# Optimization experiments

Hardware: AMD Instinct MI355X
Metric: run time of the kernel (lower is better)

Reference implementation:

```python
import jax, jax.numpy as jnp
import numpy as np

# dims
B, NV, C, HF, WF = 2, 4, 64, 128, 232
NX, NY, NZ = 128, 128, 8
VRANGE = (-25.6, -25.6, -1.0, 25.6, 25.6, 3.0)
EPS = 1e-5


def _voxel_points():
    # voxel-center grid, ordered so that reshape(NZ, NY, NX, C) is valid (x fastest)
    dx = (VRANGE[3] - VRANGE[0]) / NX
    dy = (VRANGE[4] - VRANGE[1]) / NY
    dz = (VRANGE[5] - VRANGE[2]) / NZ
    xs = VRANGE[0] + dx * (jnp.arange(NX, dtype=jnp.float32) + 0.5)
    ys = VRANGE[1] + dy * (jnp.arange(NY, dtype=jnp.float32) + 0.5)
    zs = VRANGE[2] + dz * (jnp.arange(NZ, dtype=jnp.float32) + 0.5)
    zg, yg, xg = jnp.meshgrid(zs, ys, xs, indexing='ij')  # [NZ,NY,NX]
    return jnp.stack([xg, yg, zg], axis=-1).reshape(-1, 3)  # [N,3]


def _make_cameras():
    # 4 outward-facing cameras (front, left, back, right) in a lidar frame (x fwd, y left, z up)
    dirs = [(1.0, 0.0, 0.0), (0.0, 1.0, 0.0), (-1.0, 0.0, 0.0), (0.0, -1.0, 0.0)]
    up = np.array([0.0, 0.0, 1.0])
    l2c = np.zeros((NV, 4, 4), np.float32)
    for v, f in enumerate(dirs):
        f = np.array(f)
        xc = np.cross(f, up); xc /= np.linalg.norm(xc)  # cam right
        yc = np.cross(f, xc)                              # cam down
        R = np.stack([xc, yc, f], axis=0)                 # rows: x_c, y_c, z_c
        pos = 1.0 * f + np.array([0.0, 0.0, 1.5])
        l2c[v, :3, :3] = R
        l2c[v, :3, 3] = -R @ pos
        l2c[v, 3, 3] = 1.0
    # intrinsics directly in feature-map pixel scale
    fx = fy = 0.5 * WF
    K = np.array([[fx, 0.0, WF / 2.0], [0.0, fy, HF / 2.0], [0.0, 0.0, 1.0]], np.float32)
    cam2img = np.broadcast_to(K, (NV, 3, 3))
    return (np.broadcast_to(l2c, (B, NV, 4, 4)).copy(),
            np.broadcast_to(cam2img, (B, NV, 3, 3)).copy())


def setup_inputs() -> dict:
    key = jax.random.key(0)
    feats = jax.random.normal(key, (B, NV, C, HF, WF), dtype=jnp.float32)
    l2c, k = _make_cameras()
    return {"feats": feats, "lidar2cam": jnp.asarray(l2c), "cam2img": jnp.asarray(k)}


def _bilinear(feat, px, py):
    # feat: [C,H,W]; px,py: [N] sample coords (grid_sample align_corners=False => shift by 0.5)
    x = px - 0.5
    y = py - 0.5
    x0 = jnp.floor(x); y0 = jnp.floor(y)
    wx = x - x0; wy = y - y0
    x0i = x0.astype(jnp.int32); y0i = y0.astype(jnp.int32)

    def gather(xi, yi):
        inb = (xi >= 0) & (xi < WF) & (yi >= 0) & (yi < HF)
        xc = jnp.clip(xi, 0, WF - 1)
        yc = jnp.clip(yi, 0, HF - 1)
        return feat[:, yc, xc] * inb[None, :].astype(feat.dtype)  # [C,N]

    return (gather(x0i, y0i) * ((1 - wx) * (1 - wy))[None]
            + gather(x0i + 1, y0i) * (wx * (1 - wy))[None]
            + gather(x0i, y0i + 1) * ((1 - wx) * wy)[None]
            + gather(x0i + 1, y0i + 1) * (wx * wy)[None])


def reference(feats, lidar2cam, cam2img):
    pts = _voxel_points()                                   # [N,3]
    pts_h = jnp.concatenate([pts, jnp.ones((pts.shape[0], 1), pts.dtype)], axis=-1)  # [N,4]
    cam = jnp.einsum('bvij,nj->bvni', lidar2cam, pts_h)[..., :3]  # [B,NV,N,3]
    z = cam[..., 2]
    uvw = jnp.einsum('bvij,bvnj->bvni', cam2img, cam)
    zc = jnp.clip(z, EPS, None)
    px = uvw[..., 0] / zc
    py = uvw[..., 1] / zc
    valid = (z > EPS) & (px >= 0) & (px < WF) & (py >= 0) & (py < HF)  # [B,NV,N]

    sample = jax.vmap(jax.vmap(_bilinear))(feats, px, py)   # [B,NV,C,N]
    sample = sample * valid[:, :, None, :].astype(sample.dtype)

    vol = sample.sum(axis=1)                                 # [B,C,N] sum over views
    cnt = valid.astype(jnp.float32).sum(axis=1)              # [B,N]
    vol = vol / jnp.clip(cnt, 1.0, None)[:, None, :]         # mean over valid views (0 where none)

    # [B,C,N] -> [N,C]-style reshape(NZ,NY,NX,C).permute(3,2,1,0) per sample -> [B,C,NX,NY,NZ]
    vol = vol.transpose(0, 2, 1).reshape(B, NZ, NY, NX, C)
    vol = vol.transpose(0, 4, 3, 2, 1)                       # [B,C,NX,NY,NZ]
    return vol
```

## Files before the change

kernel.cpp:

```cpp
#include <hip/hip_runtime.h>

#define BB   2
#define NVV  4
#define CC   64
#define HFF  128
#define WFF  232
#define HW   (HFF*WFF)
#define EPSV 1e-5f

__global__ __launch_bounds__(256) void transpose_kernel(
    const float* __restrict__ feats, float* __restrict__ ft)
{
    __shared__ float lds[64][65];
    const int t   = threadIdx.x;
    const int hw0 = blockIdx.x * 64;
    const size_t sbase = (size_t)blockIdx.y * (CC * HW);

    const int lhw = t & 63, crow = t >> 6;
#pragma unroll
    for (int r = 0; r < 16; ++r) {
        const int c = crow * 16 + r;
        lds[c][lhw] = feats[sbase + (size_t)c * HW + hw0 + lhw];
    }
    __syncthreads();
    const int lc = t & 63, hrow = t >> 6;
#pragma unroll
    for (int r = 0; r < 16; ++r) {
        const int hw = hrow + 4 * r;
        ft[sbase + (size_t)(hw0 + hw) * CC + lc] = lds[lc][hw];
    }
}

__global__ __launch_bounds__(256) void bev_sample_kernel(
    const float* __restrict__ ft,
    const float* __restrict__ l2c,
    const float* __restrict__ cam2img,
    float* __restrict__ out)
{
    __shared__ __align__(16) char smem[16640];
    int4*   s_off = (int4*)smem;
    float4* s_w   = (float4*)(smem + 4096);
    int*    s_fl  = (int*)(smem + 8192);
    float*  s_t   = (float*)smem;

    const int t   = threadIdx.x;
    const int bid = blockIdx.x;
    const int b   = bid >> 11;
    const int rem = bid & 2047;
    const int xi  = rem >> 4;
    const int yz0 = (rem & 15) << 6;

    {
        const int v = t >> 6, j = t & 63;
        const int yzi = yz0 + j;
        const int yi = yzi >> 3, zi = yzi & 7;
        const float X = -25.6f + 0.4f * ((float)xi + 0.5f);
        const float Y = -25.6f + 0.4f * ((float)yi + 0.5f);
        const float Z = -1.0f  + 0.5f * ((float)zi + 0.5f);

        const float* M = l2c + ((b * NVV + v) << 4);
        const float* K = cam2img + (b * NVV + v) * 9;
        const float cx = fmaf(M[0], X, fmaf(M[1], Y, fmaf(M[2],  Z, M[3])));
        const float cy = fmaf(M[4], X, fmaf(M[5], Y, fmaf(M[6],  Z, M[7])));
        const float cz = fmaf(M[8], X, fmaf(M[9], Y, fmaf(M[10], Z, M[11])));
        const float u = fmaf(K[0], cx, fmaf(K[1], cy, K[2] * cz));
        const float w = fmaf(K[3], cx, fmaf(K[4], cy, K[5] * cz));
        const float zc = fmaxf(cz, EPSV);
        const float rz = 1.f / zc;
        const float px = u * rz, py = w * rz;

        const bool valid = (cz > EPSV) && (px >= 0.f) && (px < (float)WFF)
                         && (py >= 0.f) && (py < (float)HFF);

        const float xf = px - 0.5f, yf = py - 0.5f;
        const float x0f = floorf(xf), y0f = floorf(yf);
        const float wx = xf - x0f, wy = yf - y0f;
        const int x0 = (int)x0f, y0 = (int)y0f;
        const int x1 = x0 + 1, y1 = y0 + 1;
        const bool bx0 = (x0 >= 0) & (x0 < WFF);
        const bool bx1 = (x1 >= 0) & (x1 < WFF);
        const bool by0 = (y0 >= 0) & (y0 < HFF);
        const bool by1 = (y1 >= 0) & (y1 < HFF);
        float4 wt;
        wt.x = (bx0 && by0) ? (1.f - wx) * (1.f - wy) : 0.f;
        wt.y = (bx1 && by0) ? wx * (1.f - wy)         : 0.f;
        wt.z = (bx0 && by1) ? (1.f - wx) * wy         : 0.f;
        wt.w = (bx1 && by1) ? wx * wy                 : 0.f;
        const int x0c = min(max(x0, 0), WFF-1), x1c = min(max(x1, 0), WFF-1);
        const int y0c = min(max(y0, 0), HFF-1), y1c = min(max(y1, 0), HFF-1);
        int4 off;
        off.x = y0c*WFF + x0c; off.y = y0c*WFF + x1c;
        off.z = y1c*WFF + x0c; off.w = y1c*WFF + x1c;

        s_off[v*64 + j] = off;
        s_w  [v*64 + j] = wt;
        ((char*)(smem + 8192))[j*4 + v] = valid ? 1 : 0;
    }
    __syncthreads();

    const int wv = t >> 6, c = t & 63;
    float acc[16];
#pragma unroll
    for (int k = 0; k < 16; ++k) acc[k] = 0.f;

    const float* fslice0 = ft + (size_t)(b * NVV) * (HW * CC);
#pragma unroll
    for (int k = 0; k < 16; ++k) {
        const int j = wv*16 + k;
        const int flags = s_fl[j];
        const int cnt = (flags & 1) + ((flags >> 8) & 1)
                      + ((flags >> 16) & 1) + ((flags >> 24) & 1);
        float a = 0.f;
#pragma unroll
        for (int v = 0; v < NVV; ++v) {
            if ((flags >> (8*v)) & 1) {
                const int4   off = s_off[v*64 + j];
                const float4 wt  = s_w  [v*64 + j];
                const float* fb  = fslice0 + (size_t)v * (HW * CC);
                a = fmaf(fb[(size_t)off.x*CC + c], wt.x, a);
                a = fmaf(fb[(size_t)off.y*CC + c], wt.y, a);
                a = fmaf(fb[(size_t)off.z*CC + c], wt.z, a);
                a = fmaf(fb[(size_t)off.w*CC + c], wt.w, a);
            }
        }
        const float scale = (cnt <= 1) ? 1.f : (cnt == 2) ? 0.5f
                          : (cnt == 3) ? (1.f/3.f) : 0.25f;
        acc[k] = a * scale;
    }
    __syncthreads();

#pragma unroll
    for (int k = 0; k < 16; ++k)
        s_t[(wv*16 + k)*65 + c] = acc[k];
    __syncthreads();

    const int jv = t & 63, cr = t >> 6;
    float* ob = out + (size_t)b * (CC * 131072) + (size_t)xi * 1024 + yz0;
#pragma unroll
    for (int r = 0; r < 16; ++r) {
        const int c2 = cr + 4*r;
        ob[(size_t)c2 * 131072 + jv] = s_t[jv*65 + c2];
    }
}

#define CG 16
__global__ __launch_bounds__(256) void bev_fuse_kernel(
    const float* __restrict__ feats, const float* __restrict__ l2c,
    const float* __restrict__ cam2img, float* __restrict__ out)
{
    const int tid = blockIdx.x * 256 + threadIdx.x;
    const int b   = tid >> 17;
    const int rem = tid & 131071;
    const int xi  = rem >> 10;
    const int yzi = rem & 1023;
    const int yi  = yzi >> 3;
    const int zi  = yzi & 7;
    const int c0  = blockIdx.y * CG;

    const float X = -25.6f + 0.4f * ((float)xi + 0.5f);
    const float Y = -25.6f + 0.4f * ((float)yi + 0.5f);
    const float Z = -1.0f  + 0.5f * ((float)zi + 0.5f);

    float acc[CG];
#pragma unroll
    for (int c = 0; c < CG; ++c) acc[c] = 0.f;
    float cnt = 0.f;

    for (int v = 0; v < NVV; ++v) {
        const float* M = l2c + ((b * NVV + v) << 4);
        const float* K = cam2img + (b * NVV + v) * 9;
        const float cx = fmaf(M[0], X, fmaf(M[1], Y, fmaf(M[2],  Z, M[3])));
        const float cy = fmaf(M[4], X, fmaf(M[5], Y, fmaf(M[6],  Z, M[7])));
        const float cz = fmaf(M[8], X, fmaf(M[9], Y, fmaf(M[10], Z, M[11])));
        const float u = fmaf(K[0], cx, fmaf(K[1], cy, K[2] * cz));
        const float w = fmaf(K[3], cx, fmaf(K[4], cy, K[5] * cz));
        const float zc = fmaxf(cz, EPSV);
        const float rz = 1.f / zc;
        const float px = u * rz, py = w * rz;
        const bool valid = (cz > EPSV) && (px >= 0.f) && (px < (float)WFF)
                         && (py >= 0.f) && (py < (float)HFF);
        if (!valid) continue;
        cnt += 1.f;
        const float xf = px - 0.5f, yf = py - 0.5f;
        const float x0f = floorf(xf), y0f = floorf(yf);
        const float wx = xf - x0f, wy = yf - y0f;
        const int x0 = (int)x0f, y0 = (int)y0f;
        const int x1 = x0 + 1, y1 = y0 + 1;
        const bool bx0 = (x0 >= 0) & (x0 < WFF);
        const bool bx1 = (x1 >= 0) & (x1 < WFF);
        const bool by0 = (y0 >= 0) & (y0 < HFF);
        const bool by1 = (y1 >= 0) & (y1 < HFF);
        const float w00 = (bx0 && by0) ? (1.f - wx) * (1.f - wy) : 0.f;
        const float w01 = (bx1 && by0) ? wx * (1.f - wy)         : 0.f;
        const float w10 = (bx0 && by1) ? (1.f - wx) * wy         : 0.f;
        const float w11 = (bx1 && by1) ? wx * wy                 : 0.f;
        const int x0c = min(max(x0,0),WFF-1), x1c = min(max(x1,0),WFF-1);
        const int y0c = min(max(y0,0),HFF-1), y1c = min(max(y1,0),HFF-1);
        const int o00 = y0c*WFF+x0c, o01 = y0c*WFF+x1c;
        const int o10 = y1c*WFF+x0c, o11 = y1c*WFF+x1c;
        const float* fb = feats + (size_t)(b*NVV+v)*(CC*HW) + (size_t)c0*HW;
#pragma unroll
        for (int c = 0; c < CG; ++c) {
            const float* fc = fb + c * HW;
            float a = acc[c];
            a = fmaf(fc[o00], w00, a);
            a = fmaf(fc[o01], w01, a);
            a = fmaf(fc[o10], w10, a);
            a = fmaf(fc[o11], w11, a);
            acc[c] = a;
        }
    }
    const float scale = 1.f / fmaxf(cnt, 1.f);
    float* ob = out + (size_t)b*(CC*131072) + (size_t)c0*131072 + xi*1024 + yzi;
#pragma unroll
    for (int c = 0; c < CG; ++c)
        ob[(size_t)c * 131072] = acc[c] * scale;
}

extern "C" void kernel_launch(void* const* d_in, const int* in_sizes, int n_in,
                              void* d_out, int out_size, void* d_ws, size_t ws_size,
                              hipStream_t stream) {
    const float* feats   = (const float*)d_in[0];
    const float* l2c     = (const float*)d_in[1];
    const float* cam2img = (const float*)d_in[2];
    float* out           = (float*)d_out;

    const size_t need = (size_t)BB * NVV * HW * CC * sizeof(float);
    if (ws_size >= need) {
        float* ft = (float*)d_ws;
        dim3 gA(HW / 64, BB * NVV, 1);
        transpose_kernel<<<gA, 256, 0, stream>>>(feats, ft);
        bev_sample_kernel<<<4096, 256, 0, stream>>>(ft, l2c, cam2img, out);
    } else {
        dim3 grid(1024, CC / CG, 1);
        bev_fuse_kernel<<<grid, 256, 0, stream>>>(feats, l2c, cam2img, out);
    }
}
```

Before: 146.7 us.

## Vectorize transpose and fetch horizontally adjacent bilinear taps as paired float2 loads

The transpose kernel now reads and writes float4 vectors instead of scalars. The sampling kernel exploits the [HW][C] layout: the two horizontal neighbour pixels are contiguous, so each half-wave loads one pixel's 64 channels as float2. The two halves are then combined with a cross-lane shuffle, and the x-edge weights are folded into a clamped base column. Voxels with no valid view skip all loads. This halves the number of gather instructions and addresses per sample, at the cost of extra shuffle work and a more intricate boundary-weight scheme.

```diff
diff --git a/kernel.cpp b/kernel.cpp
--- a/kernel.cpp
+++ b/kernel.cpp
@@ -15,19 +15,27 @@
     const int t   = threadIdx.x;
     const int hw0 = blockIdx.x * 64;
     const size_t sbase = (size_t)blockIdx.y * (CC * HW);
-
-    const int lhw = t & 63, crow = t >> 6;
-#pragma unroll
-    for (int r = 0; r < 16; ++r) {
-        const int c = crow * 16 + r;
-        lds[c][lhw] = feats[sbase + (size_t)c * HW + hw0 + lhw];
-    }
-    __syncthreads();
-    const int lc = t & 63, hrow = t >> 6;
-#pragma unroll
-    for (int r = 0; r < 16; ++r) {
-        const int hw = hrow + 4 * r;
-        ft[sbase + (size_t)(hw0 + hw) * CC + lc] = lds[lc][hw];
+    const int l16 = t & 15, g16 = t >> 4;
+
+#pragma unroll
+    for (int r = 0; r < 4; ++r) {
+        const int c = g16 + 16 * r;
+        const float4 v = *(const float4*)(feats + sbase + (size_t)c * HW + hw0 + 4 * l16);
+        lds[c][4*l16 + 0] = v.x;
+        lds[c][4*l16 + 1] = v.y;
+        lds[c][4*l16 + 2] = v.z;
+        lds[c][4*l16 + 3] = v.w;
+    }
+    __syncthreads();
+#pragma unroll
+    for (int r = 0; r < 4; ++r) {
+        const int hw = g16 + 16 * r;
+        float4 v;
+        v.x = lds[4*l16 + 0][hw];
+        v.y = lds[4*l16 + 1][hw];
+        v.z = lds[4*l16 + 2][hw];
+        v.w = lds[4*l16 + 3][hw];
+        *(float4*)(ft + sbase + (size_t)(hw0 + hw) * CC + 4 * l16) = v;
     }
 }
 
@@ -37,10 +45,10 @@
     const float* __restrict__ cam2img,
     float* __restrict__ out)
 {
-    __shared__ __align__(16) char smem[16640];
-    int4*   s_off = (int4*)smem;
-    float4* s_w   = (float4*)(smem + 4096);
-    int*    s_fl  = (int*)(smem + 8192);
+    __shared__ __align__(16) char smem[64 * 66 * 4];
+    float4* s_w   = (float4*)smem;
+    int2*   s_off = (int2*)(smem + 4096);
+    int*    s_fl  = (int*)(smem + 6144);
     float*  s_t   = (float*)smem;
 
     const int t   = threadIdx.x;
@@ -76,62 +84,79 @@
         const float x0f = floorf(xf), y0f = floorf(yf);
         const float wx = xf - x0f, wy = yf - y0f;
         const int x0 = (int)x0f, y0 = (int)y0f;
-        const int x1 = x0 + 1, y1 = y0 + 1;
-        const bool bx0 = (x0 >= 0) & (x0 < WFF);
-        const bool bx1 = (x1 >= 0) & (x1 < WFF);
-        const bool by0 = (y0 >= 0) & (y0 < HFF);
-        const bool by1 = (y1 >= 0) & (y1 < HFF);
+        const int y1 = y0 + 1;
+
+        const int bx = min(max(x0, 0), WFF - 2);
+        float wLx, wHx;
+        if (x0 < 0)            { wLx = wx;       wHx = 0.f; }
+        else if (x0 >= WFF-1)  { wLx = 0.f;      wHx = 1.f - wx; }
+        else                   { wLx = 1.f - wx; wHx = wx; }
+
+        const float ay0 = (y0 >= 0)      ? (1.f - wy) : 0.f;
+        const float ay1 = (y1 <= HFF-1)  ? wy         : 0.f;
+        const int y0c = max(y0, 0);
+        const int y1c = min(y1, HFF - 1);
+
         float4 wt;
-        wt.x = (bx0 && by0) ? (1.f - wx) * (1.f - wy) : 0.f;
-        wt.y = (bx1 && by0) ? wx * (1.f - wy)         : 0.f;
-        wt.z = (bx0 && by1) ? (1.f - wx) * wy         : 0.f;
-        wt.w = (bx1 && by1) ? wx * wy                 : 0.f;
-        const int x0c = min(max(x0, 0), WFF-1), x1c = min(max(x1, 0), WFF-1);
-        const int y0c = min(max(y0, 0), HFF-1), y1c = min(max(y1, 0), HFF-1);
-        int4 off;
-        off.x = y0c*WFF + x0c; off.y = y0c*WFF + x1c;
-        off.z = y1c*WFF + x0c; off.w = y1c*WFF + x1c;
-
+        wt.x = wLx * ay0; wt.y = wHx * ay0;
+        wt.z = wLx * ay1; wt.w = wHx * ay1;
+        int2 off;
+        off.x = y0c * WFF + bx;
+        off.y = y1c * WFF + bx;
+
+        s_w  [v*64 + j] = wt;
         s_off[v*64 + j] = off;
-        s_w  [v*64 + j] = wt;
-        ((char*)(smem + 8192))[j*4 + v] = valid ? 1 : 0;
-    }
-    __syncthreads();
-
-    const int wv = t >> 6, c = t & 63;
-    float acc[16];
-#pragma unroll
-    for (int k = 0; k < 16; ++k) acc[k] = 0.f;
-
-    const float* fslice0 = ft + (size_t)(b * NVV) * (HW * CC);
+        ((char*)(smem + 6144))[j*4 + v] = valid ? 1 : 0;
+    }
+    __syncthreads();
+
+    const int wv = t >> 6, lane = t & 63;
+    const int half = lane >> 5;
+    float2 acc[16];
+#pragma unroll
+    for (int k = 0; k < 16; ++k) acc[k] = make_float2(0.f, 0.f);
+
+    const float* fsl = ft + (size_t)(b * NVV) * (HW * CC);
 #pragma unroll
     for (int k = 0; k < 16; ++k) {
         const int j = wv*16 + k;
         const int flags = s_fl[j];
-        const int cnt = (flags & 1) + ((flags >> 8) & 1)
-                      + ((flags >> 16) & 1) + ((flags >> 24) & 1);
-        float a = 0.f;
-#pragma unroll
-        for (int v = 0; v < NVV; ++v) {
-            if ((flags >> (8*v)) & 1) {
-                const int4   off = s_off[v*64 + j];
-                const float4 wt  = s_w  [v*64 + j];
-                const float* fb  = fslice0 + (size_t)v * (HW * CC);
-                a = fmaf(fb[(size_t)off.x*CC + c], wt.x, a);
-                a = fmaf(fb[(size_t)off.y*CC + c], wt.y, a);
-                a = fmaf(fb[(size_t)off.z*CC + c], wt.z, a);
-                a = fmaf(fb[(size_t)off.w*CC + c], wt.w, a);
+        if (flags) {
+            const int cnt = (flags & 1) + ((flags >> 8) & 1)
+                          + ((flags >> 16) & 1) + ((flags >> 24) & 1);
+            float ax = 0.f, ay = 0.f;
+#pragma unroll
+            for (int v = 0; v < NVV; ++v) {
+                if ((flags >> (8*v)) & 1) {
+                    const int2   off = s_off[v*64 + j];
+                    const float4 wt  = s_w  [v*64 + j];
+                    const float* p0  = fsl + (size_t)v * (HW * CC);
+                    const float2 f0 = *(const float2*)(p0 + (size_t)off.x * CC + 2*lane);
+                    const float2 f1 = *(const float2*)(p0 + (size_t)off.y * CC + 2*lane);
+                    const float wa = half ? wt.y : wt.x;
+                    const float wb = half ? wt.w : wt.z;
+                    ax = fmaf(f0.x, wa, ax); ay = fmaf(f0.y, wa, ay);
+                    ax = fmaf(f1.x, wb, ax); ay = fmaf(f1.y, wb, ay);
+                }
             }
+            const float scale = (cnt <= 1) ? 1.f : (cnt == 2) ? 0.5f
+                              : (cnt == 3) ? (1.f/3.f) : 0.25f;
+            acc[k].x = ax * scale;
+            acc[k].y = ay * scale;
         }
-        const float scale = (cnt <= 1) ? 1.f : (cnt == 2) ? 0.5f
-                          : (cnt == 3) ? (1.f/3.f) : 0.25f;
-        acc[k] = a * scale;
-    }
-    __syncthreads();
-
-#pragma unroll
-    for (int k = 0; k < 16; ++k)
-        s_t[(wv*16 + k)*65 + c] = acc[k];
+    }
+    __syncthreads();
+
+    const int m2 = (lane & 31) * 2;
+#pragma unroll
+    for (int k = 0; k < 16; ++k) {
+        const float sx = acc[k].x + __shfl_xor(acc[k].x, 32);
+        const float sy = acc[k].y + __shfl_xor(acc[k].y, 32);
+        if ((k >> 3) == half) {
+            float2* dst = (float2*)&s_t[(wv*16 + k)*66 + m2];
+            *dst = make_float2(sx, sy);
+        }
+    }
     __syncthreads();
 
     const int jv = t & 63, cr = t >> 6;
@@ -139,7 +164,7 @@
 #pragma unroll
     for (int r = 0; r < 16; ++r) {
         const int c2 = cr + 4*r;
-        ob[(size_t)c2 * 131072 + jv] = s_t[jv*65 + c2];
+        ob[(size_t)c2 * 131072 + jv] = s_t[jv*66 + c2];
     }
 }
 
```

New measurement: 143.5 us. 2.2% less time.
